# Performance work log

Measured on AMD Instinct MI355X. Metric: run time of the kernel, lower is better.

## Reference

```python
import jax, jax.numpy as jnp
import numpy as np
import math

PI = math.pi
TWO_PI = 2.0 * math.pi
RESCALE = 2.0 * math.pi  # stand-in for dataset.rescale(FdFoRefAngle): normalized -> radians


def clamp_angle(angle):
    # |angle| mod 2pi, folded into [0, pi]
    a = jnp.abs(angle) % TWO_PI
    return jnp.where(a > PI, TWO_PI - a, a)


def setup_inputs() -> dict:
    key = jax.random.key(0)
    k1, k2 = jax.random.split(key)
    B = 8388608
    prediction = jax.random.normal(k1, (B, 3), dtype=jnp.float32)
    label = jax.random.normal(k2, (B, 3), dtype=jnp.float32)
    return {"prediction": prediction, "label": label}


def reference(prediction, label):
    pred_angle = prediction[:, 2] * RESCALE
    label_angle = label[:, 2] * RESCALE
    angle_diff = clamp_angle(pred_angle - label_angle) / PI  # [B]
    angle_diff = angle_diff[:, None]                          # [B, 1]
    pred_vector = jnp.concatenate([prediction[:, :2], angle_diff], axis=1)   # [B, 3]
    label_vector = jnp.concatenate([label[:, :2], jnp.zeros_like(angle_diff)], axis=1)
    # MSELoss(reduction='sum')
    return jnp.sum((pred_vector - label_vector) ** 2)
```

## Files before the change

### kernel.cpp

```cpp
#include <hip/hip_runtime.h>

constexpr int TPB  = 256;
constexpr int TPB2 = 1024;

__device__ __forceinline__ float row_contrib(float4 pv, float4 lv, int m) {
    const float* pp = (const float*)&pv;
    const float* ll = (const float*)&lv;
    float acc = 0.0f;
#pragma unroll
    for (int k = 0; k < 4; ++k) {
        float d = pp[k] - ll[k];
        float x = fabsf(d);
        float f = x - floorf(x);
        float t = 2.0f * fminf(f, 1.0f - f);
        bool ang = (((m + k) % 3) == 2);
        float v = ang ? t : d;
        acc = fmaf(v, v, acc);
    }
    return acc;
}

__global__ __launch_bounds__(TPB) void loss_partial_kernel(
    const float* __restrict__ pred,
    const float* __restrict__ lab,
    float* __restrict__ partial,
    long long n4,
    long long n_elems)
{
    const long long tid = (long long)blockIdx.x * blockDim.x + threadIdx.x;
    const long long S   = (long long)gridDim.x * blockDim.x;

    const float4* __restrict__ p4 = (const float4*)pred;
    const float4* __restrict__ l4 = (const float4*)lab;

    float acc = 0.0f;

    const long long q0 = tid;
    const long long q1 = tid + S;

    if (q1 < n4) {
        float4 pa = p4[q0];
        float4 la = l4[q0];
        float4 pb = p4[q1];
        float4 lb = l4[q1];
        acc += row_contrib(pa, la, (int)(q0 % 3));
        acc += row_contrib(pb, lb, (int)(q1 % 3));
        for (long long q = tid + 2 * S; q < n4; q += S) {
            float4 pv = p4[q];
            float4 lv = l4[q];
            acc += row_contrib(pv, lv, (int)(q % 3));
        }
    } else if (q0 < n4) {
        float4 pv = p4[q0];
        float4 lv = l4[q0];
        acc += row_contrib(pv, lv, (int)(q0 % 3));
    }

    const long long tail_base = n4 * 4;
    if (tid < n_elems - tail_base) {
        long long e = tail_base + tid;
        float d = pred[e] - lab[e];
        if ((int)(e % 3) == 2) {
            float x = fabsf(d);
            float f = x - floorf(x);
            d = 2.0f * fminf(f, 1.0f - f);
        }
        acc = fmaf(d, d, acc);
    }

#pragma unroll
    for (int off = 32; off > 0; off >>= 1)
        acc += __shfl_down(acc, off, 64);

    __shared__ float s_partial[TPB / 64];
    const int lane = threadIdx.x & 63;
    const int wave = threadIdx.x >> 6;
    if (lane == 0) s_partial[wave] = acc;
    __syncthreads();

    if (threadIdx.x == 0) {
        float v = 0.0f;
#pragma unroll
        for (int w = 0; w < TPB / 64; ++w) v += s_partial[w];
        partial[blockIdx.x] = v;
    }
}

__global__ __launch_bounds__(TPB2) void reduce_partials_kernel(
    const float* __restrict__ partial, float* __restrict__ out, int n)
{
    float acc = 0.0f;
    const int n4p = n / 4;
    const float4* __restrict__ p4 = (const float4*)partial;
    for (int i = threadIdx.x; i < n4p; i += TPB2) {
        float4 v = p4[i];
        acc += (v.x + v.y) + (v.z + v.w);
    }
    for (int i = n4p * 4 + threadIdx.x; i < n; i += TPB2)
        acc += partial[i];

#pragma unroll
    for (int off = 32; off > 0; off >>= 1)
        acc += __shfl_down(acc, off, 64);

    __shared__ float s_partial[TPB2 / 64];
    const int lane = threadIdx.x & 63;
    const int wave = threadIdx.x >> 6;
    if (lane == 0) s_partial[wave] = acc;
    __syncthreads();

    if (threadIdx.x == 0) {
        float v = 0.0f;
#pragma unroll
        for (int w = 0; w < TPB2 / 64; ++w) v += s_partial[w];
        out[0] = v;
    }
}

extern "C" void kernel_launch(void* const* d_in, const int* in_sizes, int n_in,
                              void* d_out, int out_size, void* d_ws, size_t ws_size,
                              hipStream_t stream) {
    const float* pred = (const float*)d_in[0];
    const float* lab  = (const float*)d_in[1];
    float* out = (float*)d_out;
    float* partial = (float*)d_ws;

    long long n_elems = (long long)in_sizes[0];
    long long n4 = n_elems / 4;

    int blocks = (int)((n4 + 2LL * TPB - 1) / (2LL * TPB));
    if (blocks < 1) blocks = 1;

    loss_partial_kernel<<<blocks, TPB, 0, stream>>>(pred, lab, partial, n4, n_elems);
    reduce_partials_kernel<<<1, TPB2, 0, stream>>>(partial, out, blocks);
}
```

Baseline: 213.3 us.

## Use fixed persistent grid with 4-way unrolled loads and incremental mod-3 phase

Replaces the data-sized grid (about 12k blocks, two float4 rows per thread) with a fixed 2048-block grid-stride loop. Each iteration issues eight float4 loads before doing any arithmetic, and it tracks the mod-3 phase by decrementing a counter instead of computing a 64-bit modulo per vector. Indexing moves to 32-bit ints. The aim is more memory-level parallelism per thread, less integer overhead and fewer partials to reduce. The cost is that each thread holds more registers, and the hardcoded grid relies on S % 3 == 2 and on n4 fitting in an int.

```diff
diff --git a/kernel.cpp b/kernel.cpp
--- a/kernel.cpp
+++ b/kernel.cpp
@@ -1,11 +1,15 @@
 #include <hip/hip_runtime.h>
 
-constexpr int TPB  = 256;
-constexpr int TPB2 = 1024;
+constexpr int TPB    = 256;
+constexpr int BLOCKS = 2048;
+constexpr int S      = BLOCKS * TPB;
+constexpr int TPB2   = 1024;
+static_assert(S % 3 == 2, "phase-decrement trick assumes S % 3 == 2");
 
-__device__ __forceinline__ float row_contrib(float4 pv, float4 lv, int m) {
-    const float* pp = (const float*)&pv;
-    const float* ll = (const float*)&lv;
+__device__ __forceinline__ float f4_contrib(float4 p, float4 l, int c) {
+    const float* pp = (const float*)&p;
+    const float* ll = (const float*)&l;
+    constexpr int want[4] = {2, 1, 0, 2};
     float acc = 0.0f;
 #pragma unroll
     for (int k = 0; k < 4; ++k) {
@@ -13,51 +17,65 @@
         float x = fabsf(d);
         float f = x - floorf(x);
         float t = 2.0f * fminf(f, 1.0f - f);
-        bool ang = (((m + k) % 3) == 2);
-        float v = ang ? t : d;
+        float v = (c == want[k]) ? t : d;
         acc = fmaf(v, v, acc);
     }
     return acc;
 }
 
-__global__ __launch_bounds__(TPB) void loss_partial_kernel(
+__device__ __forceinline__ int dec3(int c) {
+    return (c == 0) ? 2 : (c - 1);
+}
+
+__global__ __launch_bounds__(TPB, 8) void loss_partial_kernel(
     const float* __restrict__ pred,
     const float* __restrict__ lab,
     float* __restrict__ partial,
-    long long n4,
+    int n4,
     long long n_elems)
 {
-    const long long tid = (long long)blockIdx.x * blockDim.x + threadIdx.x;
-    const long long S   = (long long)gridDim.x * blockDim.x;
+    const int tid = blockIdx.x * TPB + threadIdx.x;
 
     const float4* __restrict__ p4 = (const float4*)pred;
     const float4* __restrict__ l4 = (const float4*)lab;
 
     float acc = 0.0f;
+    int c = tid % 3;
+    int q = tid;
 
-    const long long q0 = tid;
-    const long long q1 = tid + S;
+    const int iters = n4 / (4 * S);
+    for (int it = 0; it < iters; ++it) {
+        float4 pa = p4[q];
+        float4 pb = p4[q + S];
+        float4 pc = p4[q + 2 * S];
+        float4 pd = p4[q + 3 * S];
+        float4 la = l4[q];
+        float4 lb = l4[q + S];
+        float4 lc = l4[q + 2 * S];
+        float4 ld = l4[q + 3 * S];
 
-    if (q1 < n4) {
-        float4 pa = p4[q0];
-        float4 la = l4[q0];
-        float4 pb = p4[q1];
-        float4 lb = l4[q1];
-        acc += row_contrib(pa, la, (int)(q0 % 3));
-        acc += row_contrib(pb, lb, (int)(q1 % 3));
-        for (long long q = tid + 2 * S; q < n4; q += S) {
-            float4 pv = p4[q];
-            float4 lv = l4[q];
-            acc += row_contrib(pv, lv, (int)(q % 3));
-        }
-    } else if (q0 < n4) {
-        float4 pv = p4[q0];
-        float4 lv = l4[q0];
-        acc += row_contrib(pv, lv, (int)(q0 % 3));
+        const int c0 = c;
+        const int c1 = dec3(c0);
+        const int c2 = dec3(c1);
+        const int c3 = dec3(c2);
+
+        acc += f4_contrib(pa, la, c0);
+        acc += f4_contrib(pb, lb, c1);
+        acc += f4_contrib(pc, lc, c2);
+        acc += f4_contrib(pd, ld, c3);
+
+        q += 4 * S;
+        c = dec3(c3);
     }
 
-    const long long tail_base = n4 * 4;
-    if (tid < n_elems - tail_base) {
+    for (; q < n4; q += S) {
+        float4 pv = p4[q];
+        float4 lv = l4[q];
+        acc += f4_contrib(pv, lv, q % 3);
+    }
+
+    const long long tail_base = (long long)n4 * 4;
+    if (tid < (int)(n_elems - tail_base)) {
         long long e = tail_base + tid;
         float d = pred[e] - lab[e];
         if ((int)(e % 3) == 2) {
@@ -126,11 +144,8 @@
     float* partial = (float*)d_ws;
 
     long long n_elems = (long long)in_sizes[0];
-    long long n4 = n_elems / 4;
+    int n4 = (int)(n_elems / 4);
 
-    int blocks = (int)((n4 + 2LL * TPB - 1) / (2LL * TPB));
-    if (blocks < 1) blocks = 1;
-
-    loss_partial_kernel<<<blocks, TPB, 0, stream>>>(pred, lab, partial, n4, n_elems);
-    reduce_partials_kernel<<<1, TPB2, 0, stream>>>(partial, out, blocks);
+    loss_partial_kernel<<<BLOCKS, TPB, 0, stream>>>(pred, lab, partial, n4, n_elems);
+    reduce_partials_kernel<<<1, TPB2, 0, stream>>>(partial, out, BLOCKS);
 }
```

Result: no change. 215.5 us (+1.0%).

## Use persistent grid with batched inline-asm vector loads and constant phase

Applied to the files above, without the earlier changes.

Replaces the one-element-per-thread launch with a fixed persistent grid of 1536 blocks. Each thread issues 16 outstanding dwordx4 loads per iteration through inline assembly, then waits once, to raise memory-level parallelism. Because the grid stride is a multiple of 3, the column phase is computed once per thread and no longer needs a modulo per element. The hard-coded waitcnt and asm loads take scheduling away from the compiler and raise register pressure.

```diff
diff --git a/kernel.cpp b/kernel.cpp
--- a/kernel.cpp
+++ b/kernel.cpp
@@ -1,59 +1,107 @@
 #include <hip/hip_runtime.h>
 
-constexpr int TPB  = 256;
-constexpr int TPB2 = 1024;
+typedef float f32x4 __attribute__((ext_vector_type(4)));
 
-__device__ __forceinline__ float row_contrib(float4 pv, float4 lv, int m) {
-    const float* pp = (const float*)&pv;
-    const float* ll = (const float*)&lv;
+constexpr int TPB    = 256;
+constexpr int BLOCKS = 1536;
+constexpr long long S = (long long)BLOCKS * TPB;
+constexpr int TPB2   = 1024;
+static_assert(S % 3 == 0, "constant-phase trick needs S % 3 == 0");
+
+__device__ __forceinline__ float f4_contrib(f32x4 p, f32x4 l, int c) {
+    constexpr int want[4] = {2, 1, 0, 2};
     float acc = 0.0f;
 #pragma unroll
     for (int k = 0; k < 4; ++k) {
-        float d = pp[k] - ll[k];
+        float d = p[k] - l[k];
         float x = fabsf(d);
         float f = x - floorf(x);
         float t = 2.0f * fminf(f, 1.0f - f);
-        bool ang = (((m + k) % 3) == 2);
-        float v = ang ? t : d;
+        float v = (c == want[k]) ? t : d;
         acc = fmaf(v, v, acc);
     }
     return acc;
 }
 
-__global__ __launch_bounds__(TPB) void loss_partial_kernel(
+__global__ __launch_bounds__(TPB, 4) void loss_partial_kernel(
     const float* __restrict__ pred,
     const float* __restrict__ lab,
     float* __restrict__ partial,
     long long n4,
     long long n_elems)
 {
-    const long long tid = (long long)blockIdx.x * blockDim.x + threadIdx.x;
-    const long long S   = (long long)gridDim.x * blockDim.x;
+    const long long tid = (long long)blockIdx.x * TPB + threadIdx.x;
+    const f32x4* __restrict__ p4 = (const f32x4*)pred;
+    const f32x4* __restrict__ l4 = (const f32x4*)lab;
 
-    const float4* __restrict__ p4 = (const float4*)pred;
-    const float4* __restrict__ l4 = (const float4*)lab;
-
+    const int c = (int)(tid % 3);
     float acc = 0.0f;
 
-    const long long q0 = tid;
-    const long long q1 = tid + S;
+    const long long iters = n4 / (8 * S);
+    long long base = tid;
 
-    if (q1 < n4) {
-        float4 pa = p4[q0];
-        float4 la = l4[q0];
-        float4 pb = p4[q1];
-        float4 lb = l4[q1];
-        acc += row_contrib(pa, la, (int)(q0 % 3));
-        acc += row_contrib(pb, lb, (int)(q1 % 3));
-        for (long long q = tid + 2 * S; q < n4; q += S) {
-            float4 pv = p4[q];
-            float4 lv = l4[q];
-            acc += row_contrib(pv, lv, (int)(q % 3));
-        }
-    } else if (q0 < n4) {
-        float4 pv = p4[q0];
-        float4 lv = l4[q0];
-        acc += row_contrib(pv, lv, (int)(q0 % 3));
+    for (long long it = 0; it < iters; ++it) {
+        f32x4 P[8], L[8];
+        const f32x4* ap0 = p4 + base;
+        const f32x4* ap1 = p4 + base + 1 * S;
+        const f32x4* ap2 = p4 + base + 2 * S;
+        const f32x4* ap3 = p4 + base + 3 * S;
+        const f32x4* ap4 = p4 + base + 4 * S;
+        const f32x4* ap5 = p4 + base + 5 * S;
+        const f32x4* ap6 = p4 + base + 6 * S;
+        const f32x4* ap7 = p4 + base + 7 * S;
+        const f32x4* al0 = l4 + base;
+        const f32x4* al1 = l4 + base + 1 * S;
+        const f32x4* al2 = l4 + base + 2 * S;
+        const f32x4* al3 = l4 + base + 3 * S;
+        const f32x4* al4 = l4 + base + 4 * S;
+        const f32x4* al5 = l4 + base + 5 * S;
+        const f32x4* al6 = l4 + base + 6 * S;
+        const f32x4* al7 = l4 + base + 7 * S;
+
+        asm volatile(
+            "global_load_dwordx4 %0, %16, off\n\t"
+            "global_load_dwordx4 %1, %17, off\n\t"
+            "global_load_dwordx4 %2, %18, off\n\t"
+            "global_load_dwordx4 %3, %19, off\n\t"
+            "global_load_dwordx4 %4, %20, off\n\t"
+            "global_load_dwordx4 %5, %21, off\n\t"
+            "global_load_dwordx4 %6, %22, off\n\t"
+            "global_load_dwordx4 %7, %23, off\n\t"
+            "global_load_dwordx4 %8, %24, off\n\t"
+            "global_load_dwordx4 %9, %25, off\n\t"
+            "global_load_dwordx4 %10, %26, off\n\t"
+            "global_load_dwordx4 %11, %27, off\n\t"
+            "global_load_dwordx4 %12, %28, off\n\t"
+            "global_load_dwordx4 %13, %29, off\n\t"
+            "global_load_dwordx4 %14, %30, off\n\t"
+            "global_load_dwordx4 %15, %31, off"
+            : "=&v"(P[0]), "=&v"(P[1]), "=&v"(P[2]), "=&v"(P[3]),
+              "=&v"(P[4]), "=&v"(P[5]), "=&v"(P[6]), "=&v"(P[7]),
+              "=&v"(L[0]), "=&v"(L[1]), "=&v"(L[2]), "=&v"(L[3]),
+              "=&v"(L[4]), "=&v"(L[5]), "=&v"(L[6]), "=&v"(L[7])
+            : "v"(ap0), "v"(ap1), "v"(ap2), "v"(ap3),
+              "v"(ap4), "v"(ap5), "v"(ap6), "v"(ap7),
+              "v"(al0), "v"(al1), "v"(al2), "v"(al3),
+              "v"(al4), "v"(al5), "v"(al6), "v"(al7));
+
+        asm volatile("s_waitcnt vmcnt(0)"
+            : "+v"(P[0]), "+v"(P[1]), "+v"(P[2]), "+v"(P[3]),
+              "+v"(P[4]), "+v"(P[5]), "+v"(P[6]), "+v"(P[7]),
+              "+v"(L[0]), "+v"(L[1]), "+v"(L[2]), "+v"(L[3]),
+              "+v"(L[4]), "+v"(L[5]), "+v"(L[6]), "+v"(L[7]));
+
+#pragma unroll
+        for (int k = 0; k < 8; ++k)
+            acc += f4_contrib(P[k], L[k], c);
+
+        base += 8 * S;
+    }
+
+    for (long long q = iters * 8 * S + tid; q < n4; q += S) {
+        f32x4 pv = p4[q];
+        f32x4 lv = l4[q];
+        acc += f4_contrib(pv, lv, (int)(q % 3));
     }
 
     const long long tail_base = n4 * 4;
@@ -128,9 +176,6 @@
     long long n_elems = (long long)in_sizes[0];
     long long n4 = n_elems / 4;
 
-    int blocks = (int)((n4 + 2LL * TPB - 1) / (2LL * TPB));
-    if (blocks < 1) blocks = 1;
-
-    loss_partial_kernel<<<blocks, TPB, 0, stream>>>(pred, lab, partial, n4, n_elems);
-    reduce_partials_kernel<<<1, TPB2, 0, stream>>>(partial, out, blocks);
+    loss_partial_kernel<<<BLOCKS, TPB, 0, stream>>>(pred, lab, partial, n4, n_elems);
+    reduce_partials_kernel<<<1, TPB2, 0, stream>>>(partial, out, BLOCKS);
 }
```

Result: no change. 212.9 us (-0.2%).
